# Performance work log

Measured on AMD Instinct MI355X. Metric: run time of the kernel, lower is better.

Reference implementation:

```python
import jax, jax.numpy as jnp
import numpy as np

T, H, E, I = 1024, 2048, 64, 1024          # tokens, hidden, routed experts, expert ffn dim
N_GROUP, TOPK_GROUP, TOP_K = 8, 4, 8
N_SHARED = 2
ROUTED_SCALE = 2.5
IS = I * N_SHARED                            # shared-expert intermediate size


def setup_inputs() -> dict:
    key = jax.random.key(0)
    ks = jax.random.split(key, 8)
    s = 0.02
    return {
        "hidden_states": jax.random.normal(ks[0], (T, H), jnp.float32),
        "gate_w": jax.random.normal(ks[1], (E, H), jnp.float32) * s,
        "e_bias": jax.random.normal(ks[2], (E,), jnp.float32) * s,
        "w_gate": jax.random.normal(ks[3], (E, I, H), jnp.float32) * s,
        "w_up": jax.random.normal(ks[4], (E, I, H), jnp.float32) * s,
        "w_down": jax.random.normal(ks[5], (E, H, I), jnp.float32) * s,
        "shared_w_gate_up": jax.random.normal(ks[6], (2 * IS, H), jnp.float32) * s,
        "shared_w_down": jax.random.normal(ks[7], (H, IS), jnp.float32) * s,
    }


def _grouped_topk(scores, bias):
    """DeepSeek noaux_tc grouped top-k: sigmoid scores + correction bias,
    pick top `TOPK_GROUP` groups by sum of their top-2 biased scores,
    then top-K experts among allowed groups; weights from unbiased scores."""
    Tn, En = scores.shape
    s = scores + bias[None, :]                                   # [T, E]
    g = s.reshape(Tn, N_GROUP, En // N_GROUP)                    # [T, G, E/G]
    group_scores = jnp.sum(jax.lax.top_k(g, 2)[0], axis=-1)      # [T, G]
    _, gidx = jax.lax.top_k(group_scores, TOPK_GROUP)            # [T, topk_group]
    gmask = jnp.zeros((Tn, N_GROUP), scores.dtype).at[
        jnp.arange(Tn)[:, None], gidx].set(1.0)                  # [T, G]
    smask = jnp.repeat(gmask, En // N_GROUP, axis=1)             # [T, E]
    masked = jnp.where(smask > 0, s, -jnp.inf)
    _, topk_ids = jax.lax.top_k(masked, TOP_K)                   # [T, K]
    w = jnp.take_along_axis(scores, topk_ids, axis=1)            # unbiased scores
    w = w / jnp.sum(w, axis=-1, keepdims=True)                   # renormalize (norm_topk_prob)
    return w, topk_ids


def reference(hidden_states, gate_w, e_bias, w_gate, w_up, w_down,
              shared_w_gate_up, shared_w_down):
    x = hidden_states                                            # [T, H]
    router_logits = x @ gate_w.T                                 # [T, E]
    scores = jax.nn.sigmoid(router_logits)
    topk_w, topk_ids = _grouped_topk(scores, e_bias)             # [T, K] each
    # sparse combine weights [T, E] (zero for unselected experts)
    cw = jnp.zeros((x.shape[0], E), x.dtype).at[
        jnp.arange(x.shape[0])[:, None], topk_ids].add(topk_w)
    # routed experts: dense grouped-GEMM form of the fused-MoE math
    g = jnp.einsum('th,eih->tei', x, w_gate)                     # [T, E, I]
    u = jnp.einsum('th,eih->tei', x, w_up)
    h = jax.nn.silu(g) * u
    routed = jnp.einsum('tei,te,ehi->th', h, cw, w_down)         # [T, H]
    # shared experts MLP (SiluAndMul)
    sg_u = x @ shared_w_gate_up.T                                # [T, 2*IS]
    sg, su = jnp.split(sg_u, 2, axis=-1)
    shared = (jax.nn.silu(sg) * su) @ shared_w_down.T            # [T, H]
    return routed * ROUTED_SCALE + shared
```

## Files before the change

kernel.cpp:

```cpp
#include <hip/hip_runtime.h>
#include <hip/hip_bf16.h>
#include <math.h>

#define T_TOK 1024
#define HID   2048
#define NEXP  64
#define IDIM  1024
#define ISH   2048
#define TOPK  8

typedef float  f32x4  __attribute__((ext_vector_type(4)));
typedef __bf16 bf16x8 __attribute__((ext_vector_type(8)));

#define BM  64
#define BN_ 64
#define BK  64

#define BARRIER_NODRAIN() asm volatile("s_waitcnt lgkmcnt(0)\n\ts_barrier" ::: "memory")

__device__ __forceinline__ bf16x8 cvt8(f32x4 a, f32x4 b) {
  bf16x8 v;
  v[0]=(__bf16)a[0]; v[1]=(__bf16)a[1]; v[2]=(__bf16)a[2]; v[3]=(__bf16)a[3];
  v[4]=(__bf16)b[0]; v[5]=(__bf16)b[1]; v[6]=(__bf16)b[2]; v[7]=(__bf16)b[3];
  return v;
}

__global__ void init_kernel(int* counts) {
  if (threadIdx.x < NEXP) counts[threadIdx.x] = 0;
}

__global__ void xcast_kernel(const float* __restrict__ x, __bf16* __restrict__ xb) {
  long i = ((long)blockIdx.x * 256 + threadIdx.x) * 8;
  f32x4 a = *(const f32x4*)(x + i);
  f32x4 b = *(const f32x4*)(x + i + 4);
  *(bf16x8*)(xb + i) = cvt8(a, b);
}

__global__ __launch_bounds__(256)
void router_kernel(const float* __restrict__ x, const float* __restrict__ gw,
                   const float* __restrict__ eb,
                   int* __restrict__ ids, float* __restrict__ wts,
                   int* __restrict__ counts)
{
  __shared__ __align__(16) float xs[HID];
  __shared__ float red[256];
  __shared__ float sc[NEXP], sb[NEXP];
  const int t = blockIdx.x, tid = threadIdx.x;

  const f32x4* xsrc = (const f32x4*)(x + (long)t * HID);
  f32x4* xd = (f32x4*)xs;
  xd[tid]       = xsrc[tid];
  xd[tid + 256] = xsrc[tid + 256];
  __syncthreads();

  const int e = tid & 63, part = tid >> 6;
  const f32x4* wrow = (const f32x4*)(gw + (long)e * HID + part * 512);
  const f32x4* xrow = (const f32x4*)(xs + part * 512);
  float s = 0.f;
  #pragma unroll 4
  for (int j = 0; j < 128; ++j) {
    f32x4 wv = wrow[j], xv = xrow[j];
    s += wv[0]*xv[0] + wv[1]*xv[1] + wv[2]*xv[2] + wv[3]*xv[3];
  }
  red[tid] = s;
  __syncthreads();
  if (part == 0) {
    float logit = red[e] + red[e+64] + red[e+128] + red[e+192];
    float sig = 1.f / (1.f + expf(-logit));
    sc[e] = sig; sb[e] = sig + eb[e];
  }
  __syncthreads();

  if (tid == 0) {
    float gsc[8];
    for (int g = 0; g < 8; ++g) {
      float m1 = -1e30f, m2 = -1e30f;
      for (int j = 0; j < 8; ++j) {
        float v = sb[g*8 + j];
        if (v > m1) { m2 = m1; m1 = v; } else if (v > m2) m2 = v;
      }
      gsc[g] = m1 + m2;
    }
    unsigned gmask = 0;
    for (int it = 0; it < 4; ++it) {
      int best = 0; float bv = -1e30f;
      for (int g = 0; g < 8; ++g)
        if (!((gmask >> g) & 1) && gsc[g] > bv) { bv = gsc[g]; best = g; }
      gmask |= 1u << best;
    }
    unsigned long long taken = 0;
    int id8[8]; float wsum = 0.f;
    for (int it = 0; it < 8; ++it) {
      int best = 0; float bv = -1e30f;
      for (int e2 = 0; e2 < 64; ++e2) {
        if (!((gmask >> (e2 >> 3)) & 1)) continue;
        if ((taken >> e2) & 1) continue;
        float v = sb[e2];
        if (v > bv) { bv = v; best = e2; }
      }
      taken |= 1ull << best;
      id8[it] = best; wsum += sc[best];
    }
    float inv = 2.5f / wsum;
    for (int k = 0; k < 8; ++k) {
      ids[t*8 + k] = id8[k];
      wts[t*8 + k] = sc[id8[k]] * inv;
      atomicAdd(&counts[id8[k]], 1);
    }
  }
}

__global__ void scan_kernel(const int* __restrict__ counts,
                            int* __restrict__ seg_off, int* __restrict__ cursors,
                            int* __restrict__ pair_e, int* __restrict__ pair_mt,
                            int* __restrict__ npairs) {
  if (threadIdx.x == 0) {
    int off = 0, np = 0;
    for (int e = 0; e < NEXP; ++e) {
      seg_off[e] = off; cursors[e] = off;
      int c = counts[e]; off += c;
      for (int m = 0; m * BM < c; ++m) { pair_e[np] = e; pair_mt[np] = m; ++np; }
    }
    npairs[0] = np;
  }
}

__global__ void scatter_kernel(const int* __restrict__ ids, const float* __restrict__ wts,
                               int* __restrict__ cursors,
                               int* __restrict__ tok_list, float* __restrict__ wgt_list,
                               int* __restrict__ pos_of) {
  int idx = blockIdx.x * 256 + threadIdx.x;
  if (idx >= T_TOK * TOPK) return;
  int t = idx >> 3;
  int e = ids[idx];
  int pos = atomicAdd(&cursors[e], 1);
  tok_list[pos] = t;
  wgt_list[pos] = wts[idx];
  pos_of[idx] = pos;
}

template<bool ROUTED>
__global__ __launch_bounds__(256, 3)
void gu_kernel(const __bf16* __restrict__ A, const float* __restrict__ Bg0,
               const float* __restrict__ Bu0, long strideBe, int ldB, int K,
               __bf16* __restrict__ Hout, int ldh,
               const int* __restrict__ pair_e, const int* __restrict__ pair_mt,
               const int* __restrict__ npairs,
               const int* __restrict__ seg_off, const int* __restrict__ seg_cnt,
               const int* __restrict__ tok_list, const float* __restrict__ wgt_list,
               int Mfull)
{
  const int tid  = threadIdx.x;
  const int lane = tid & 63;
  const int wv   = tid >> 6;

  int e, mt0, soff, cnt;
  if (ROUTED) {
    int p = blockIdx.y;
    if (p >= npairs[0]) return;
    e = pair_e[p]; mt0 = pair_mt[p]; soff = seg_off[e]; cnt = seg_cnt[e];
  } else {
    e = 0; mt0 = blockIdx.y; soff = 0; cnt = Mfull;
  }
  const int rem = cnt - mt0 * BM;
  if (rem <= 0) return;

  const long bcol = (long)(blockIdx.x * BN_ + wv * 16 + (lane & 15));
  const float* Bg = Bg0 + (long)e * strideBe + bcol * ldB + ((lane >> 4) * 8);
  const float* Bu = Bu0 + (long)e * strideBe + bcol * ldB + ((lane >> 4) * 8);

  __shared__ __align__(16) __bf16 Abuf[2][BM * BK];
  __shared__ float Ws[BM];

  const __bf16* aptr[2];
  int aoff[2];
  #pragma unroll
  for (int i = 0; i < 2; ++i) {
    int c = tid + i * 256, r = c >> 3, s = c & 7;
    int rr = (r < rem) ? r : (rem - 1);
    int base = soff + mt0 * BM + rr;
    int arow = ROUTED ? tok_list[base] : base;
    aptr[i] = A + (long)arow * K + s * 8;
    aoff[i] = r * 64 + ((s ^ (r & 7)) * 8);
  }

  f32x4 ag[4] = {}, au[4] = {};
  bf16x8 aR[2];
  f32x4 gA[4], gB[4], uA[4], uB[4];

#define LOAD_A(k) { _Pragma("unroll") \
  for (int i = 0; i < 2; ++i) aR[i] = *(const bf16x8*)(aptr[i] + (k)); }
#define STORE_A(b) { _Pragma("unroll") \
  for (int i = 0; i < 2; ++i) *(bf16x8*)&Abuf[b][aoff[i]] = aR[i]; }
#define LOAD_BP(ptr, dst, k) { \
  dst[0] = *(const f32x4*)(ptr + (k));      dst[1] = *(const f32x4*)(ptr + (k) + 4); \
  dst[2] = *(const f32x4*)(ptr + (k) + 32); dst[3] = *(const f32x4*)(ptr + (k) + 36); }
#define COMPUTE(gs, us, b) { _Pragma("unroll") \
  for (int ch = 0; ch < 2; ++ch) { \
    bf16x8 bg = cvt8(gs[ch*2], gs[ch*2+1]); \
    bf16x8 bu = cvt8(us[ch*2], us[ch*2+1]); \
    const int ro = ((lane & 15) * 64) + ((((ch*4) + (lane >> 4)) ^ (lane & 7)) * 8); \
    _Pragma("unroll") \
    for (int m = 0; m < 4; ++m) { \
      bf16x8 af = *(const bf16x8*)&Abuf[b][m * 1024 + ro]; \
      ag[m] = __builtin_amdgcn_mfma_f32_16x16x32_bf16(af, bg, ag[m], 0, 0, 0); \
      au[m] = __builtin_amdgcn_mfma_f32_16x16x32_bf16(af, bu, au[m], 0, 0, 0); \
    } \
  } }

  LOAD_A(0);
  LOAD_BP(Bg, gA, 0); LOAD_BP(Bu, uA, 0);
  const int NT = K / BK;
  for (int t = 0; t < NT; t += 2) {
    const int k1 = (t + 1 < NT) ? (t + 1) * BK : 0;
    const int k2 = (t + 2 < NT) ? (t + 2) * BK : 0;
    STORE_A(0);
    LOAD_A(k1); LOAD_BP(Bg, gB, k1); LOAD_BP(Bu, uB, k1);
    BARRIER_NODRAIN();
    COMPUTE(gA, uA, 0);
    STORE_A(1);
    LOAD_A(k2); LOAD_BP(Bg, gA, k2); LOAD_BP(Bu, uA, k2);
    BARRIER_NODRAIN();
    COMPUTE(gB, uB, 1);
  }
#undef LOAD_A
#undef STORE_A
#undef LOAD_BP
#undef COMPUTE

  if (tid < BM) {
    int rr = (tid < rem) ? tid : (rem - 1);
    Ws[tid] = ROUTED ? wgt_list[soff + mt0 * BM + rr] : 1.f;
  }
  __syncthreads();
  __bf16* Cs = &Abuf[0][0];
  #pragma unroll
  for (int m = 0; m < 4; ++m) {
    #pragma unroll
    for (int r = 0; r < 4; ++r) {
      int row = m * 16 + (lane >> 4) * 4 + r;
      float g = ag[m][r], u = au[m][r];
      float h = Ws[row] * g * u / (1.f + __expf(-g));
      Cs[row * 64 + wv * 16 + (lane & 15)] = (__bf16)h;
    }
  }
  __syncthreads();
  {
    int row = tid >> 2;
    if (row < rem) {
      __bf16* dst = Hout + (long)(soff + mt0 * BM + row) * ldh + blockIdx.x * BN_;
      #pragma unroll
      for (int j = 0; j < 2; ++j) {
        int c8 = (tid & 3) * 2 + j;
        *(bf16x8*)(dst + c8 * 8) = *(const bf16x8*)&Cs[row * 64 + c8 * 8];
      }
    }
  }
}

template<int EPI>
__global__ __launch_bounds__(256, 4)
void down_kernel(const __bf16* __restrict__ A, const float* __restrict__ B0,
                 long strideBe, int ldB, int K, void* __restrict__ Out, int ldc,
                 const int* __restrict__ pair_e, const int* __restrict__ pair_mt,
                 const int* __restrict__ npairs,
                 const int* __restrict__ seg_off, const int* __restrict__ seg_cnt,
                 int Mfull)
{
  const int tid  = threadIdx.x;
  const int lane = tid & 63;
  const int wv   = tid >> 6;

  int e, mt0, soff, cnt;
  if (EPI == 1) {
    int p = blockIdx.y;
    if (p >= npairs[0]) return;
    e = pair_e[p]; mt0 = pair_mt[p]; soff = seg_off[e]; cnt = seg_cnt[e];
  } else {
    e = 0; mt0 = blockIdx.y; soff = 0; cnt = Mfull;
  }
  const int rem = cnt - mt0 * BM;
  if (rem <= 0) return;

  const long bcol = (long)(blockIdx.x * BN_ + wv * 16 + (lane & 15));
  const float* Bp = B0 + (long)e * strideBe + bcol * ldB + ((lane >> 4) * 8);

  __shared__ __align__(16) __bf16 Abuf[2][BM * BK];

  const __bf16* aptr[2];
  int aoff[2];
  #pragma unroll
  for (int i = 0; i < 2; ++i) {
    int c = tid + i * 256, r = c >> 3, s = c & 7;
    int rr = (r < rem) ? r : (rem - 1);
    aptr[i] = A + (long)(soff + mt0 * BM + rr) * K + s * 8;
    aoff[i] = r * 64 + ((s ^ (r & 7)) * 8);
  }

  f32x4 acc[4] = {};
  bf16x8 aR[2];
  f32x4 bA[4], bB[4];

#define LOAD_A(k) { _Pragma("unroll") \
  for (int i = 0; i < 2; ++i) aR[i] = *(const bf16x8*)(aptr[i] + (k)); }
#define STORE_A(b) { _Pragma("unroll") \
  for (int i = 0; i < 2; ++i) *(bf16x8*)&Abuf[b][aoff[i]] = aR[i]; }
#define LOAD_B(dst, k) { \
  dst[0] = *(const f32x4*)(Bp + (k));      dst[1] = *(const f32x4*)(Bp + (k) + 4); \
  dst[2] = *(const f32x4*)(Bp + (k) + 32); dst[3] = *(const f32x4*)(Bp + (k) + 36); }
#define COMPUTE(bs, b) { _Pragma("unroll") \
  for (int ch = 0; ch < 2; ++ch) { \
    bf16x8 bfrag = cvt8(bs[ch*2], bs[ch*2+1]); \
    const int ro = ((lane & 15) * 64) + ((((ch*4) + (lane >> 4)) ^ (lane & 7)) * 8); \
    _Pragma("unroll") \
    for (int m = 0; m < 4; ++m) { \
      bf16x8 af = *(const bf16x8*)&Abuf[b][m * 1024 + ro]; \
      acc[m] = __builtin_amdgcn_mfma_f32_16x16x32_bf16(af, bfrag, acc[m], 0, 0, 0); \
    } \
  } }

  LOAD_A(0);
  LOAD_B(bA, 0);
  const int NT = K / BK;
  for (int t = 0; t < NT; t += 2) {
    const int k1 = (t + 1 < NT) ? (t + 1) * BK : 0;
    const int k2 = (t + 2 < NT) ? (t + 2) * BK : 0;
    STORE_A(0);
    LOAD_A(k1); LOAD_B(bB, k1);
    BARRIER_NODRAIN();
    COMPUTE(bA, 0);
    STORE_A(1);
    LOAD_A(k2); LOAD_B(bA, k2);
    BARRIER_NODRAIN();
    COMPUTE(bB, 1);
  }
#undef LOAD_A
#undef STORE_A
#undef LOAD_B
#undef COMPUTE

  if (EPI == 1) {
    __syncthreads();
    __bf16* Cs = &Abuf[0][0];
    #pragma unroll
    for (int m = 0; m < 4; ++m) {
      #pragma unroll
      for (int r = 0; r < 4; ++r) {
        int row = m * 16 + (lane >> 4) * 4 + r;
        Cs[row * 64 + wv * 16 + (lane & 15)] = (__bf16)acc[m][r];
      }
    }
    __syncthreads();
    int row = tid >> 2;
    if (row < rem) {
      __bf16* dst = (__bf16*)Out + (long)(soff + mt0 * BM + row) * ldc + blockIdx.x * BN_;
      #pragma unroll
      for (int j = 0; j < 2; ++j) {
        int c8 = (tid & 3) * 2 + j;
        *(bf16x8*)(dst + c8 * 8) = *(const bf16x8*)&Cs[row * 64 + c8 * 8];
      }
    }
  } else {
    float* O = (float*)Out;
    const int col = blockIdx.x * BN_ + wv * 16 + (lane & 15);
    #pragma unroll
    for (int m = 0; m < 4; ++m) {
      #pragma unroll
      for (int r = 0; r < 4; ++r) {
        int row = m * 16 + (lane >> 4) * 4 + r;
        if (row < rem)
          O[(long)(mt0 * BM + row) * ldc + col] = acc[m][r];
      }
    }
  }
}

__global__ __launch_bounds__(256)
void combine_kernel(const __bf16* __restrict__ y, const int* __restrict__ pos_of,
                    float* __restrict__ out) {
  const int t = blockIdx.x;
  const int c0 = threadIdx.x * 8;
  float* orow = out + (long)t * HID + c0;
  f32x4 s0 = *(const f32x4*)orow;
  f32x4 s1 = *(const f32x4*)(orow + 4);
  #pragma unroll
  for (int k = 0; k < TOPK; ++k) {
    int row = pos_of[t * TOPK + k];
    bf16x8 v = *(const bf16x8*)(y + (long)row * HID + c0);
    s0[0] += (float)v[0]; s0[1] += (float)v[1]; s0[2] += (float)v[2]; s0[3] += (float)v[3];
    s1[0] += (float)v[4]; s1[1] += (float)v[5]; s1[2] += (float)v[6]; s1[3] += (float)v[7];
  }
  *(f32x4*)orow = s0;
  *(f32x4*)(orow + 4) = s1;
}

extern "C" void kernel_launch(void* const* d_in, const int* in_sizes, int n_in,
                              void* d_out, int out_size, void* d_ws, size_t ws_size,
                              hipStream_t stream) {
  const float* x      = (const float*)d_in[0];
  const float* gate_w = (const float*)d_in[1];
  const float* e_bias = (const float*)d_in[2];
  const float* w_gate = (const float*)d_in[3];
  const float* w_up   = (const float*)d_in[4];
  const float* w_down = (const float*)d_in[5];
  const float* sw_gu  = (const float*)d_in[6];
  const float* sw_d   = (const float*)d_in[7];
  float* out = (float*)d_out;
  char* ws = (char*)d_ws;

  size_t off = 0;
  __bf16* x_bf = (__bf16*)(ws + off);        off += (size_t)T_TOK * HID * 2;
  int*    ids  = (int*)(ws + off);           off += T_TOK * TOPK * 4;
  float*  wts  = (float*)(ws + off);         off += T_TOK * TOPK * 4;
  int* counts  = (int*)(ws + off);           off += 256;
  int* segoff  = (int*)(ws + off);           off += 256;
  int* cursors = (int*)(ws + off);           off += 256;
  int* pair_e  = (int*)(ws + off);           off += 1024;
  int* pair_mt = (int*)(ws + off);           off += 1024;
  int* npairs  = (int*)(ws + off);           off += 256;
  int* tok_list = (int*)(ws + off);          off += T_TOK * TOPK * 4;
  float* wgt_list = (float*)(ws + off);      off += T_TOK * TOPK * 4;
  int* pos_of  = (int*)(ws + off);           off += T_TOK * TOPK * 4;
  off = (off + 255) & ~(size_t)255;
  __bf16* h_buf  = (__bf16*)(ws + off);      off += (size_t)T_TOK * TOPK * IDIM * 2;
  __bf16* hs_buf = (__bf16*)(ws + off);      off += (size_t)T_TOK * ISH * 2;
  __bf16* y_buf  = (__bf16*)(ws + off);      off += (size_t)T_TOK * TOPK * HID * 2;

  init_kernel<<<1, 64, 0, stream>>>(counts);
  xcast_kernel<<<(T_TOK * HID) / (256 * 8), 256, 0, stream>>>(x, x_bf);
  router_kernel<<<T_TOK, 256, 0, stream>>>(x, gate_w, e_bias, ids, wts, counts);
  scan_kernel<<<1, 64, 0, stream>>>(counts, segoff, cursors, pair_e, pair_mt, npairs);
  scatter_kernel<<<(T_TOK * TOPK + 255) / 256, 256, 0, stream>>>(
      ids, wts, cursors, tok_list, wgt_list, pos_of);

  gu_kernel<true><<<dim3(IDIM / BN_, 256), 256, 0, stream>>>(
      x_bf, w_gate, w_up, (long)IDIM * HID, HID, HID, h_buf, IDIM,
      pair_e, pair_mt, npairs, segoff, counts, tok_list, wgt_list, 0);

  gu_kernel<false><<<dim3(ISH / BN_, T_TOK / BM), 256, 0, stream>>>(
      x_bf, sw_gu, sw_gu + (size_t)ISH * HID, 0, HID, HID, hs_buf, ISH,
      nullptr, nullptr, nullptr, nullptr, nullptr, nullptr, nullptr, T_TOK);

  down_kernel<2><<<dim3(HID / BN_, T_TOK / BM), 256, 0, stream>>>(
      hs_buf, sw_d, 0, ISH, ISH, out, HID,
      nullptr, nullptr, nullptr, nullptr, nullptr, T_TOK);

  down_kernel<1><<<dim3(HID / BN_, 256), 256, 0, stream>>>(
      h_buf, w_down, (long)HID * IDIM, IDIM, IDIM, y_buf, HID,
      pair_e, pair_mt, npairs, segoff, counts, 0);

  combine_kernel<<<T_TOK, 256, 0, stream>>>(y_buf, pos_of, out);
}
```

Before: 783.6 us.

## Double M tile, split gate/up GEMMs across grid z, move SiLU-mul to separate kernel

Result: faster. 674.9 us (-13.9%).

```diff
diff --git a/kernel.cpp b/kernel.cpp
--- a/kernel.cpp
+++ b/kernel.cpp
@@ -12,7 +12,7 @@
 typedef float  f32x4  __attribute__((ext_vector_type(4)));
 typedef __bf16 bf16x8 __attribute__((ext_vector_type(8)));
 
-#define BM  64
+#define BM  128
 #define BN_ 64
 #define BK  64
 
@@ -141,14 +141,15 @@
 
 template<bool ROUTED>
 __global__ __launch_bounds__(256, 3)
-void gu_kernel(const __bf16* __restrict__ A, const float* __restrict__ Bg0,
-               const float* __restrict__ Bu0, long strideBe, int ldB, int K,
-               __bf16* __restrict__ Hout, int ldh,
-               const int* __restrict__ pair_e, const int* __restrict__ pair_mt,
-               const int* __restrict__ npairs,
-               const int* __restrict__ seg_off, const int* __restrict__ seg_cnt,
-               const int* __restrict__ tok_list, const float* __restrict__ wgt_list,
-               int Mfull)
+void gu2_kernel(const __bf16* __restrict__ A,
+                const float* __restrict__ Bg0, const float* __restrict__ Bu0,
+                long strideBe, int ldB, int K,
+                __bf16* __restrict__ Cg, __bf16* __restrict__ Cu, int ldc,
+                const int* __restrict__ pair_e, const int* __restrict__ pair_mt,
+                const int* __restrict__ npairs,
+                const int* __restrict__ seg_off, const int* __restrict__ seg_cnt,
+                const int* __restrict__ tok_list,
+                int Mfull)
 {
   const int tid  = threadIdx.x;
   const int lane = tid & 63;
@@ -165,17 +166,19 @@
   const int rem = cnt - mt0 * BM;
   if (rem <= 0) return;
 
-  const long bcol = (long)(blockIdx.x * BN_ + wv * 16 + (lane & 15));
-  const float* Bg = Bg0 + (long)e * strideBe + bcol * ldB + ((lane >> 4) * 8);
-  const float* Bu = Bu0 + (long)e * strideBe + bcol * ldB + ((lane >> 4) * 8);
+  const float* B0 = blockIdx.z ? Bu0 : Bg0;
+  __bf16* Cout    = blockIdx.z ? Cu  : Cg;
+
+  const float* Bp = B0 + (long)e * strideBe
+                  + (long)(blockIdx.x * BN_ + wv * 16 + (lane & 15)) * ldB
+                  + ((lane >> 4) * 8);
 
   __shared__ __align__(16) __bf16 Abuf[2][BM * BK];
-  __shared__ float Ws[BM];
-
-  const __bf16* aptr[2];
-  int aoff[2];
-  #pragma unroll
-  for (int i = 0; i < 2; ++i) {
+
+  const __bf16* aptr[4];
+  int aoff[4];
+  #pragma unroll
+  for (int i = 0; i < 4; ++i) {
     int c = tid + i * 256, r = c >> 3, s = c & 7;
     int rr = (r < rem) ? r : (rem - 1);
     int base = soff + mt0 * BM + rr;
@@ -184,136 +187,23 @@
     aoff[i] = r * 64 + ((s ^ (r & 7)) * 8);
   }
 
-  f32x4 ag[4] = {}, au[4] = {};
-  bf16x8 aR[2];
-  f32x4 gA[4], gB[4], uA[4], uB[4];
+  f32x4 acc[8] = {};
+  bf16x8 aR[4];
+  f32x4 bA[4], bB[4];
 
 #define LOAD_A(k) { _Pragma("unroll") \
-  for (int i = 0; i < 2; ++i) aR[i] = *(const bf16x8*)(aptr[i] + (k)); }
+  for (int i = 0; i < 4; ++i) aR[i] = *(const bf16x8*)(aptr[i] + (k)); }
 #define STORE_A(b) { _Pragma("unroll") \
-  for (int i = 0; i < 2; ++i) *(bf16x8*)&Abuf[b][aoff[i]] = aR[i]; }
-#define LOAD_BP(ptr, dst, k) { \
-  dst[0] = *(const f32x4*)(ptr + (k));      dst[1] = *(const f32x4*)(ptr + (k) + 4); \
-  dst[2] = *(const f32x4*)(ptr + (k) + 32); dst[3] = *(const f32x4*)(ptr + (k) + 36); }
-#define COMPUTE(gs, us, b) { _Pragma("unroll") \
-  for (int ch = 0; ch < 2; ++ch) { \
-    bf16x8 bg = cvt8(gs[ch*2], gs[ch*2+1]); \
-    bf16x8 bu = cvt8(us[ch*2], us[ch*2+1]); \
-    const int ro = ((lane & 15) * 64) + ((((ch*4) + (lane >> 4)) ^ (lane & 7)) * 8); \
-    _Pragma("unroll") \
-    for (int m = 0; m < 4; ++m) { \
-      bf16x8 af = *(const bf16x8*)&Abuf[b][m * 1024 + ro]; \
-      ag[m] = __builtin_amdgcn_mfma_f32_16x16x32_bf16(af, bg, ag[m], 0, 0, 0); \
-      au[m] = __builtin_amdgcn_mfma_f32_16x16x32_bf16(af, bu, au[m], 0, 0, 0); \
-    } \
-  } }
-
-  LOAD_A(0);
-  LOAD_BP(Bg, gA, 0); LOAD_BP(Bu, uA, 0);
-  const int NT = K / BK;
-  for (int t = 0; t < NT; t += 2) {
-    const int k1 = (t + 1 < NT) ? (t + 1) * BK : 0;
-    const int k2 = (t + 2 < NT) ? (t + 2) * BK : 0;
-    STORE_A(0);
-    LOAD_A(k1); LOAD_BP(Bg, gB, k1); LOAD_BP(Bu, uB, k1);
-    BARRIER_NODRAIN();
-    COMPUTE(gA, uA, 0);
-    STORE_A(1);
-    LOAD_A(k2); LOAD_BP(Bg, gA, k2); LOAD_BP(Bu, uA, k2);
-    BARRIER_NODRAIN();
-    COMPUTE(gB, uB, 1);
-  }
-#undef LOAD_A
-#undef STORE_A
-#undef LOAD_BP
-#undef COMPUTE
-
-  if (tid < BM) {
-    int rr = (tid < rem) ? tid : (rem - 1);
-    Ws[tid] = ROUTED ? wgt_list[soff + mt0 * BM + rr] : 1.f;
-  }
-  __syncthreads();
-  __bf16* Cs = &Abuf[0][0];
-  #pragma unroll
-  for (int m = 0; m < 4; ++m) {
-    #pragma unroll
-    for (int r = 0; r < 4; ++r) {
-      int row = m * 16 + (lane >> 4) * 4 + r;
-      float g = ag[m][r], u = au[m][r];
-      float h = Ws[row] * g * u / (1.f + __expf(-g));
-      Cs[row * 64 + wv * 16 + (lane & 15)] = (__bf16)h;
-    }
-  }
-  __syncthreads();
-  {
-    int row = tid >> 2;
-    if (row < rem) {
-      __bf16* dst = Hout + (long)(soff + mt0 * BM + row) * ldh + blockIdx.x * BN_;
-      #pragma unroll
-      for (int j = 0; j < 2; ++j) {
-        int c8 = (tid & 3) * 2 + j;
-        *(bf16x8*)(dst + c8 * 8) = *(const bf16x8*)&Cs[row * 64 + c8 * 8];
-      }
-    }
-  }
-}
-
-template<int EPI>
-__global__ __launch_bounds__(256, 4)
-void down_kernel(const __bf16* __restrict__ A, const float* __restrict__ B0,
-                 long strideBe, int ldB, int K, void* __restrict__ Out, int ldc,
-                 const int* __restrict__ pair_e, const int* __restrict__ pair_mt,
-                 const int* __restrict__ npairs,
-                 const int* __restrict__ seg_off, const int* __restrict__ seg_cnt,
-                 int Mfull)
-{
-  const int tid  = threadIdx.x;
-  const int lane = tid & 63;
-  const int wv   = tid >> 6;
-
-  int e, mt0, soff, cnt;
-  if (EPI == 1) {
-    int p = blockIdx.y;
-    if (p >= npairs[0]) return;
-    e = pair_e[p]; mt0 = pair_mt[p]; soff = seg_off[e]; cnt = seg_cnt[e];
-  } else {
-    e = 0; mt0 = blockIdx.y; soff = 0; cnt = Mfull;
-  }
-  const int rem = cnt - mt0 * BM;
-  if (rem <= 0) return;
-
-  const long bcol = (long)(blockIdx.x * BN_ + wv * 16 + (lane & 15));
-  const float* Bp = B0 + (long)e * strideBe + bcol * ldB + ((lane >> 4) * 8);
-
-  __shared__ __align__(16) __bf16 Abuf[2][BM * BK];
-
-  const __bf16* aptr[2];
-  int aoff[2];
-  #pragma unroll
-  for (int i = 0; i < 2; ++i) {
-    int c = tid + i * 256, r = c >> 3, s = c & 7;
-    int rr = (r < rem) ? r : (rem - 1);
-    aptr[i] = A + (long)(soff + mt0 * BM + rr) * K + s * 8;
-    aoff[i] = r * 64 + ((s ^ (r & 7)) * 8);
-  }
-
-  f32x4 acc[4] = {};
-  bf16x8 aR[2];
-  f32x4 bA[4], bB[4];
-
-#define LOAD_A(k) { _Pragma("unroll") \
-  for (int i = 0; i < 2; ++i) aR[i] = *(const bf16x8*)(aptr[i] + (k)); }
-#define STORE_A(b) { _Pragma("unroll") \
-  for (int i = 0; i < 2; ++i) *(bf16x8*)&Abuf[b][aoff[i]] = aR[i]; }
+  for (int i = 0; i < 4; ++i) *(bf16x8*)&Abuf[b][aoff[i]] = aR[i]; }
 #define LOAD_B(dst, k) { \
   dst[0] = *(const f32x4*)(Bp + (k));      dst[1] = *(const f32x4*)(Bp + (k) + 4); \
   dst[2] = *(const f32x4*)(Bp + (k) + 32); dst[3] = *(const f32x4*)(Bp + (k) + 36); }
-#define COMPUTE(bs, b) { _Pragma("unroll") \
+#define COMPUTE(bsrc, b) { _Pragma("unroll") \
   for (int ch = 0; ch < 2; ++ch) { \
-    bf16x8 bfrag = cvt8(bs[ch*2], bs[ch*2+1]); \
+    bf16x8 bfrag = cvt8(bsrc[ch*2], bsrc[ch*2+1]); \
     const int ro = ((lane & 15) * 64) + ((((ch*4) + (lane >> 4)) ^ (lane & 7)) * 8); \
     _Pragma("unroll") \
-    for (int m = 0; m < 4; ++m) { \
+    for (int m = 0; m < 8; ++m) { \
       bf16x8 af = *(const bf16x8*)&Abuf[b][m * 1024 + ro]; \
       acc[m] = __builtin_amdgcn_mfma_f32_16x16x32_bf16(af, bfrag, acc[m], 0, 0, 0); \
     } \
@@ -339,11 +229,113 @@
 #undef LOAD_B
 #undef COMPUTE
 
+  __syncthreads();
+  __bf16* Cs = &Abuf[0][0];
+  #pragma unroll
+  for (int m = 0; m < 8; ++m) {
+    #pragma unroll
+    for (int r = 0; r < 4; ++r) {
+      int row = m * 16 + (lane >> 4) * 4 + r;
+      Cs[row * 64 + wv * 16 + (lane & 15)] = (__bf16)acc[m][r];
+    }
+  }
+  __syncthreads();
+  #pragma unroll
+  for (int p = 0; p < 4; ++p) {
+    int row = p * 32 + (tid >> 3);
+    if (row < rem)
+      *(bf16x8*)(Cout + (long)(soff + mt0 * BM + row) * ldc + blockIdx.x * BN_ + (tid & 7) * 8) =
+          *(const bf16x8*)&Cs[row * 64 + (tid & 7) * 8];
+  }
+}
+
+template<int EPI>
+__global__ __launch_bounds__(256, 3)
+void down_kernel(const __bf16* __restrict__ A, const float* __restrict__ B0,
+                 long strideBe, int ldB, int K, void* __restrict__ Out, int ldc,
+                 const int* __restrict__ pair_e, const int* __restrict__ pair_mt,
+                 const int* __restrict__ npairs,
+                 const int* __restrict__ seg_off, const int* __restrict__ seg_cnt,
+                 int Mfull)
+{
+  const int tid  = threadIdx.x;
+  const int lane = tid & 63;
+  const int wv   = tid >> 6;
+
+  int e, mt0, soff, cnt;
+  if (EPI == 1) {
+    int p = blockIdx.y;
+    if (p >= npairs[0]) return;
+    e = pair_e[p]; mt0 = pair_mt[p]; soff = seg_off[e]; cnt = seg_cnt[e];
+  } else {
+    e = 0; mt0 = blockIdx.y; soff = 0; cnt = Mfull;
+  }
+  const int rem = cnt - mt0 * BM;
+  if (rem <= 0) return;
+
+  const float* Bp = B0 + (long)e * strideBe
+                  + (long)(blockIdx.x * BN_ + wv * 16 + (lane & 15)) * ldB
+                  + ((lane >> 4) * 8);
+
+  __shared__ __align__(16) __bf16 Abuf[2][BM * BK];
+
+  const __bf16* aptr[4];
+  int aoff[4];
+  #pragma unroll
+  for (int i = 0; i < 4; ++i) {
+    int c = tid + i * 256, r = c >> 3, s = c & 7;
+    int rr = (r < rem) ? r : (rem - 1);
+    aptr[i] = A + (long)(soff + mt0 * BM + rr) * K + s * 8;
+    aoff[i] = r * 64 + ((s ^ (r & 7)) * 8);
+  }
+
+  f32x4 acc[8] = {};
+  bf16x8 aR[4];
+  f32x4 bA[4], bB[4];
+
+#define LOAD_A(k) { _Pragma("unroll") \
+  for (int i = 0; i < 4; ++i) aR[i] = *(const bf16x8*)(aptr[i] + (k)); }
+#define STORE_A(b) { _Pragma("unroll") \
+  for (int i = 0; i < 4; ++i) *(bf16x8*)&Abuf[b][aoff[i]] = aR[i]; }
+#define LOAD_B(dst, k) { \
+  dst[0] = *(const f32x4*)(Bp + (k));      dst[1] = *(const f32x4*)(Bp + (k) + 4); \
+  dst[2] = *(const f32x4*)(Bp + (k) + 32); dst[3] = *(const f32x4*)(Bp + (k) + 36); }
+#define COMPUTE(bs, b) { _Pragma("unroll") \
+  for (int ch = 0; ch < 2; ++ch) { \
+    bf16x8 bfrag = cvt8(bs[ch*2], bs[ch*2+1]); \
+    const int ro = ((lane & 15) * 64) + ((((ch*4) + (lane >> 4)) ^ (lane & 7)) * 8); \
+    _Pragma("unroll") \
+    for (int m = 0; m < 8; ++m) { \
+      bf16x8 af = *(const bf16x8*)&Abuf[b][m * 1024 + ro]; \
+      acc[m] = __builtin_amdgcn_mfma_f32_16x16x32_bf16(af, bfrag, acc[m], 0, 0, 0); \
+    } \
+  } }
+
+  LOAD_A(0);
+  LOAD_B(bA, 0);
+  const int NT = K / BK;
+  for (int t = 0; t < NT; t += 2) {
+    const int k1 = (t + 1 < NT) ? (t + 1) * BK : 0;
+    const int k2 = (t + 2 < NT) ? (t + 2) * BK : 0;
+    STORE_A(0);
+    LOAD_A(k1); LOAD_B(bB, k1);
+    BARRIER_NODRAIN();
+    COMPUTE(bA, 0);
+    STORE_A(1);
+    LOAD_A(k2); LOAD_B(bA, k2);
+    BARRIER_NODRAIN();
+    COMPUTE(bB, 1);
+  }
+#undef LOAD_A
+#undef STORE_A
+#undef LOAD_B
+#undef COMPUTE
+
   if (EPI == 1) {
     __syncthreads();
     __bf16* Cs = &Abuf[0][0];
     #pragma unroll
-    for (int m = 0; m < 4; ++m) {
+    for (int m = 0; m < 8; ++m) {
       #pragma unroll
       for (int r = 0; r < 4; ++r) {
         int row = m * 16 + (lane >> 4) * 4 + r;
@@ -351,20 +343,18 @@
       }
     }
     __syncthreads();
-    int row = tid >> 2;
-    if (row < rem) {
-      __bf16* dst = (__bf16*)Out + (long)(soff + mt0 * BM + row) * ldc + blockIdx.x * BN_;
-      #pragma unroll
-      for (int j = 0; j < 2; ++j) {
-        int c8 = (tid & 3) * 2 + j;
-        *(bf16x8*)(dst + c8 * 8) = *(const bf16x8*)&Cs[row * 64 + c8 * 8];
-      }
+    #pragma unroll
+    for (int p = 0; p < 4; ++p) {
+      int row = p * 32 + (tid >> 3);
+      if (row < rem)
+        *(bf16x8*)((__bf16*)Out + (long)(soff + mt0 * BM + row) * ldc + blockIdx.x * BN_ + (tid & 7) * 8) =
+            *(const bf16x8*)&Cs[row * 64 + (tid & 7) * 8];
     }
   } else {
     float* O = (float*)Out;
     const int col = blockIdx.x * BN_ + wv * 16 + (lane & 15);
     #pragma unroll
-    for (int m = 0; m < 4; ++m) {
+    for (int m = 0; m < 8; ++m) {
       #pragma unroll
       for (int r = 0; r < 4; ++r) {
         int row = m * 16 + (lane >> 4) * 4 + r;
@@ -373,6 +363,21 @@
       }
     }
   }
+}
+
+__global__ void fuse_kernel(__bf16* __restrict__ g, const __bf16* __restrict__ u,
+                            const float* __restrict__ wrow, int rshift) {
+  long idx = ((long)blockIdx.x * 256 + threadIdx.x) * 8;
+  bf16x8 gv = *(bf16x8*)(g + idx);
+  bf16x8 uv = *(const bf16x8*)(u + idx);
+  float w = wrow ? wrow[idx >> rshift] : 1.f;
+  bf16x8 h;
+  #pragma unroll
+  for (int j = 0; j < 8; ++j) {
+    float gf = (float)gv[j], uf = (float)uv[j];
+    h[j] = (__bf16)(w * gf * uf / (1.f + __expf(-gf)));
+  }
+  *(bf16x8*)(g + idx) = h;
 }
 
 __global__ __launch_bounds__(256)
@@ -422,8 +427,10 @@
   float* wgt_list = (float*)(ws + off);      off += T_TOK * TOPK * 4;
   int* pos_of  = (int*)(ws + off);           off += T_TOK * TOPK * 4;
   off = (off + 255) & ~(size_t)255;
-  __bf16* h_buf  = (__bf16*)(ws + off);      off += (size_t)T_TOK * TOPK * IDIM * 2;
-  __bf16* hs_buf = (__bf16*)(ws + off);      off += (size_t)T_TOK * ISH * 2;
+  __bf16* g_buf  = (__bf16*)(ws + off);      off += (size_t)T_TOK * TOPK * IDIM * 2;
+  __bf16* u_buf  = (__bf16*)(ws + off);      off += (size_t)T_TOK * TOPK * IDIM * 2;
+  __bf16* gs_buf = (__bf16*)(ws + off);      off += (size_t)T_TOK * ISH * 2;
+  __bf16* us_buf = (__bf16*)(ws + off);      off += (size_t)T_TOK * ISH * 2;
   __bf16* y_buf  = (__bf16*)(ws + off);      off += (size_t)T_TOK * TOPK * HID * 2;
 
   init_kernel<<<1, 64, 0, stream>>>(counts);
@@ -433,20 +440,23 @@
   scatter_kernel<<<(T_TOK * TOPK + 255) / 256, 256, 0, stream>>>(
       ids, wts, cursors, tok_list, wgt_list, pos_of);
 
-  gu_kernel<true><<<dim3(IDIM / BN_, 256), 256, 0, stream>>>(
-      x_bf, w_gate, w_up, (long)IDIM * HID, HID, HID, h_buf, IDIM,
-      pair_e, pair_mt, npairs, segoff, counts, tok_list, wgt_list, 0);
-
-  gu_kernel<false><<<dim3(ISH / BN_, T_TOK / BM), 256, 0, stream>>>(
-      x_bf, sw_gu, sw_gu + (size_t)ISH * HID, 0, HID, HID, hs_buf, ISH,
-      nullptr, nullptr, nullptr, nullptr, nullptr, nullptr, nullptr, T_TOK);
+  gu2_kernel<true><<<dim3(IDIM / BN_, 128, 2), 256, 0, stream>>>(
+      x_bf, w_gate, w_up, (long)IDIM * HID, HID, HID, g_buf, u_buf, IDIM,
+      pair_e, pair_mt, npairs, segoff, counts, tok_list, 0);
+
+  fuse_kernel<<<(T_TOK * TOPK * IDIM) / (256 * 8), 256, 0, stream>>>(g_buf, u_buf, wgt_list, 10);
+
+  gu2_kernel<false><<<dim3(ISH / BN_, T_TOK / BM, 2), 256, 0, stream>>>(
+      x_bf, sw_gu, sw_gu + (size_t)ISH * HID, 0, HID, HID, gs_buf, us_buf, ISH,
+      nullptr, nullptr, nullptr, nullptr, nullptr, nullptr, T_TOK);
+  fuse_kernel<<<(T_TOK * ISH) / (256 * 8), 256, 0, stream>>>(gs_buf, us_buf, nullptr, 11);
 
   down_kernel<2><<<dim3(HID / BN_, T_TOK / BM), 256, 0, stream>>>(
-      hs_buf, sw_d, 0, ISH, ISH, out, HID,
+      gs_buf, sw_d, 0, ISH, ISH, out, HID,
       nullptr, nullptr, nullptr, nullptr, nullptr, T_TOK);
 
-  down_kernel<1><<<dim3(HID / BN_, 256), 256, 0, stream>>>(
-      h_buf, w_down, (long)HID * IDIM, IDIM, IDIM, y_buf, HID,
+  down_kernel<1><<<dim3(HID / BN_, 128), 256, 0, stream>>>(
+      g_buf, w_down, (long)HID * IDIM, IDIM, IDIM, y_buf, HID,
       pair_e, pair_mt, npairs, segoff, counts, 0);
 
   combine_kernel<<<T_TOK, 256, 0, stream>>>(y_buf, pos_of, out);
```
